# Performance work log

Hardware: AMD Instinct MI355X
Metric: run time of the kernel (lower is better)

The kernel has to match this reference:

```python
import jax, jax.numpy as jnp
import numpy as np

B, L, D, H, HID = 2048, 512, 17, 8, 256  # batch, max entities, feat dim, heads, mlp hidden
SPECIAL, OUT = 9, 23  # special vector dims, policy logits (7+16)


def _lin(k, out_d, in_d, scale):
    kw, kb = jax.random.split(k)
    W = jax.random.normal(kw, (out_d, in_d), jnp.float32) * scale
    b = jax.random.normal(kb, (out_d,), jnp.float32) * 0.01
    return W, b


def setup_inputs() -> dict:
    key = jax.random.key(0)
    ks = jax.random.split(key, 16)
    # observations: row 0 holds the 9-dim special vector, rows 1..L are ragged entities
    x = jax.random.normal(ks[0], (B, L + 1, D), jnp.float32)
    lengths = jax.random.randint(ks[1], (B,), 1, L + 1)
    mask = (jnp.arange(L)[None, :] < lengths[:, None]).astype(jnp.float32)
    x = x.at[:, 1:, :].multiply(mask[:, :, None])  # zero rows mark padding
    s = 1.0 / np.sqrt(D)
    # per-head K/V projections (num_heads separate tiny Linears)
    Wk = jax.random.normal(ks[2], (H, D, D), jnp.float32) * s
    bk = jax.random.normal(ks[3], (H, D), jnp.float32) * 0.01
    Wv = jax.random.normal(ks[4], (H, D, D), jnp.float32) * s
    bv = jax.random.normal(ks[5], (H, D), jnp.float32) * 0.01
    q = jax.random.normal(ks[6], (H, D), jnp.float32)  # learned per-head queries
    Wo, bo = _lin(ks[7], D, H * D, 1.0 / np.sqrt(H * D))
    sc = 1.0 / np.sqrt(D + SPECIAL)
    pW1, pb1 = _lin(ks[8], HID, D + SPECIAL, sc)
    pW2, pb2 = _lin(ks[9], HID, HID, 1.0 / np.sqrt(HID))
    pW3, pb3 = _lin(ks[10], OUT, HID, 1.0 / np.sqrt(HID))
    vW1, vb1 = _lin(ks[11], HID, D + SPECIAL, sc)
    vW2, vb2 = _lin(ks[12], HID, HID, 1.0 / np.sqrt(HID))
    vW3, vb3 = _lin(ks[13], 1, HID, 1.0 / np.sqrt(HID))
    return dict(x=x, Wk=Wk, bk=bk, Wv=Wv, bv=bv, q=q, Wo=Wo, bo=bo,
                pW1=pW1, pb1=pb1, pW2=pW2, pb2=pb2, pW3=pW3, pb3=pb3,
                vW1=vW1, vb1=vb1, vW2=vW2, vb2=vb2, vW3=vW3, vb3=vb3)


def _mlp(h, W1, b1, W2, b2, W3, b3):
    h = jax.nn.relu(h @ W1.T + b1)
    h = jax.nn.relu(h @ W2.T + b2)
    return h @ W3.T + b3


def reference(x, Wk, bk, Wv, bv, q, Wo, bo,
              pW1, pb1, pW2, pb2, pW3, pb3,
              vW1, vb1, vW2, vb2, vW3, vb3):
    special = x[:, 0, :SPECIAL]            # [B, 9]
    seq = x[:, 1:, :]                      # [B, L, D]
    mask = jnp.sum(jnp.abs(seq), axis=-1) != 0  # [B, L] non-padded rows
    # per-head keys/values for all samples at once (batched over the head loop)
    keys = jnp.einsum('bld,hed->bhle', seq, Wk) + bk[None, :, None, :]   # [B,H,L,D]
    vals = jnp.einsum('bld,hed->bhle', seq, Wv) + bv[None, :, None, :]   # [B,H,L,D]
    scores = jnp.einsum('bhle,he->bhl', keys, q)                          # [B,H,L]
    scores = jnp.where(mask[:, None, :], scores, -1e9)
    w = jax.nn.softmax(scores, axis=-1)                                   # [B,H,L]
    agg = jnp.einsum('bhl,bhle->bhe', w, vals).reshape(x.shape[0], H * D)  # concat heads
    attn = agg @ Wo.T + bo                                                # [B, D]
    comb = jnp.concatenate([attn, special], axis=-1)                      # [B, D+9]
    logits = _mlp(comb, pW1, pb1, pW2, pb2, pW3, pb3)                     # [B, 23]
    value = _mlp(comb, vW1, vb1, vW2, vb2, vW3, vb3)                      # [B, 1]
    return logits, value
```

## Files before the change

kernel.cpp:

```cpp
#include <hip/hip_runtime.h>
#include <hip/hip_bf16.h>

#define B_ 2048
#define D_ 17
#define H_ 8
#define HID_ 256
#define OUT_ 23
#define XROW 8721

__device__ __forceinline__ float4 ld4u(const float* p) {
  float4 v; __builtin_memcpy(&v, p, 16); return v;
}
__device__ __forceinline__ float bclane(float v, int l) {
  return __uint_as_float(__builtin_amdgcn_readlane(__float_as_uint(v), l));
}

__global__ __launch_bounds__(256) void prep_kernel(
    const float* __restrict__ pW2, const float* __restrict__ vW2,
    const float* __restrict__ Wk, const float* __restrict__ bk,
    const float* __restrict__ q,
    float* __restrict__ pW2t, float* __restrict__ vW2t, float* __restrict__ qkc)
{
  const int bid = blockIdx.x;
  const int t = threadIdx.x;
  if (bid == 128) {
    if (t < H_ * D_) {
      const int h = t / D_, dd = t - h * D_;
      float s = 0.f;
      #pragma unroll
      for (int e = 0; e < D_; ++e) s = fmaf(Wk[h*289 + e*D_ + dd], q[h*D_ + e], s);
      qkc[h*18 + dd] = s;
    } else if (t < H_ * D_ + H_) {
      const int h = t - H_ * D_;
      float s = 0.f;
      #pragma unroll
      for (int e = 0; e < D_; ++e) s = fmaf(bk[h*D_ + e], q[h*D_ + e], s);
      qkc[h*18 + 17] = s;
    }
    return;
  }
  __shared__ float tile[32][33];
  const int m = bid >> 6, tid = bid & 63;
  const int ti = (tid >> 3) * 32, tk = (tid & 7) * 32;
  const float* src = m ? vW2 : pW2;
  float* dst = m ? vW2t : pW2t;
  const int tx = t & 31, ty = t >> 5;
  #pragma unroll
  for (int r = 0; r < 4; ++r) tile[ty + 8*r][tx] = src[(ti + ty + 8*r)*HID_ + tk + tx];
  __syncthreads();
  #pragma unroll
  for (int r = 0; r < 4; ++r) dst[(tk + ty + 8*r)*HID_ + ti + tx] = tile[tx][ty + 8*r];
}

__global__ __launch_bounds__(64) void attn_part_kernel(
    const float* __restrict__ x, const float* __restrict__ qkc,
    float* __restrict__ part)
{
  const int bid = blockIdx.x;
  const int b = bid >> 2, q = bid & 3;
  const int lane = threadIdx.x;
  const int h = lane & 7, rg = lane >> 3;
  const float* xs = x + (size_t)b * XROW + D_;
  const int r0 = q * 128;

  const float w0 = xs[(size_t)(r0 + 8 * (lane & 15)) * D_];
  const unsigned long long lv = __ballot((lane < 16) && (w0 != 0.f));
  const int nch = lv ? (64 - __builtin_clzll(lv)) : 0;

  float qk[D_];
  #pragma unroll
  for (int d = 0; d < D_; ++d) qk[d] = qkc[h*18 + d];
  const float chr = qkc[h*18 + 17];

  float den = 0.f, acc[D_];
  #pragma unroll
  for (int d = 0; d < D_; ++d) acc[d] = 0.f;

  if (nch) {
    const float* rb = xs + (size_t)(r0 + rg) * D_;
    float4 A0, A1, A2, A3; float A4;
    float4 C0, C1, C2, C3; float C4;
    auto loadA = [&](int g) {
      const float* rp = rb + g * 136;
      A0 = ld4u(rp); A1 = ld4u(rp+4); A2 = ld4u(rp+8); A3 = ld4u(rp+12); A4 = rp[16];
    };
    auto loadC = [&](int g) {
      const float* rp = rb + g * 136;
      C0 = ld4u(rp); C1 = ld4u(rp+4); C2 = ld4u(rp+8); C3 = ld4u(rp+12); C4 = rp[16];
    };
    auto comp = [&](const float4& v0, const float4& v1, const float4& v2, const float4& v3, float v4) {
      float sc = chr;
      sc = fmaf(qk[0],  v0.x, sc); sc = fmaf(qk[1],  v0.y, sc);
      sc = fmaf(qk[2],  v0.z, sc); sc = fmaf(qk[3],  v0.w, sc);
      sc = fmaf(qk[4],  v1.x, sc); sc = fmaf(qk[5],  v1.y, sc);
      sc = fmaf(qk[6],  v1.z, sc); sc = fmaf(qk[7],  v1.w, sc);
      sc = fmaf(qk[8],  v2.x, sc); sc = fmaf(qk[9],  v2.y, sc);
      sc = fmaf(qk[10], v2.z, sc); sc = fmaf(qk[11], v2.w, sc);
      sc = fmaf(qk[12], v3.x, sc); sc = fmaf(qk[13], v3.y, sc);
      sc = fmaf(qk[14], v3.z, sc); sc = fmaf(qk[15], v3.w, sc);
      sc = fmaf(qk[16], v4, sc);
      const float p = (v0.x != 0.f) ? __expf(sc) : 0.f;
      den += p;
      acc[0]  = fmaf(p, v0.x, acc[0]);  acc[1]  = fmaf(p, v0.y, acc[1]);
      acc[2]  = fmaf(p, v0.z, acc[2]);  acc[3]  = fmaf(p, v0.w, acc[3]);
      acc[4]  = fmaf(p, v1.x, acc[4]);  acc[5]  = fmaf(p, v1.y, acc[5]);
      acc[6]  = fmaf(p, v1.z, acc[6]);  acc[7]  = fmaf(p, v1.w, acc[7]);
      acc[8]  = fmaf(p, v2.x, acc[8]);  acc[9]  = fmaf(p, v2.y, acc[9]);
      acc[10] = fmaf(p, v2.z, acc[10]); acc[11] = fmaf(p, v2.w, acc[11]);
      acc[12] = fmaf(p, v3.x, acc[12]); acc[13] = fmaf(p, v3.y, acc[13]);
      acc[14] = fmaf(p, v3.z, acc[14]); acc[15] = fmaf(p, v3.w, acc[15]);
      acc[16] = fmaf(p, v4, acc[16]);
    };

    loadA(0);
    #pragma unroll 1
    for (int g = 0; g < nch; g += 2) {
      if (g + 1 < nch) loadC(g + 1);
      comp(A0, A1, A2, A3, A4);
      if (g + 1 >= nch) break;
      if (g + 2 < nch) loadA(g + 2);
      comp(C0, C1, C2, C3, C4);
    }
  }

  #pragma unroll
  for (int m = 8; m <= 32; m <<= 1) {
    den += __shfl_xor(den, m, 64);
    #pragma unroll
    for (int d = 0; d < D_; ++d) acc[d] += __shfl_xor(acc[d], m, 64);
  }
  if (lane < 8) {
    float* pp = part + (size_t)bid * 144 + lane * 18;
    pp[0] = den;
    #pragma unroll
    for (int d = 0; d < D_; ++d) pp[1 + d] = acc[d];
  }
}

__global__ __launch_bounds__(512) void mlp_fused_kernel(
    const float* __restrict__ x, const float* __restrict__ part,
    const float* __restrict__ Wv, const float* __restrict__ bv,
    const float* __restrict__ Wo, const float* __restrict__ bo,
    const float* __restrict__ pW1, const float* __restrict__ pb1,
    const float* __restrict__ pW2t, const float* __restrict__ pb2,
    const float* __restrict__ pW3, const float* __restrict__ pb3,
    const float* __restrict__ vW1, const float* __restrict__ vb1,
    const float* __restrict__ vW2t, const float* __restrict__ vb2,
    const float* __restrict__ vW3, const float* __restrict__ vb3,
    float* __restrict__ out)
{
  __shared__ float s_swn[8][136];
  __shared__ float s_agg[8][136];
  __shared__ float s_wp[8][136];
  __shared__ float s_comb[8][26];
  __shared__ __align__(16) float s_red[2][3][8][HID_];
  __shared__ __align__(16) float s_h2[2][8][HID_];

  const int t = threadIdx.x;
  const int b0 = blockIdx.x * 8;
  const int cb = t >> 6;
  const int cl = t & 63;

  {
    const float* pb_ = part + (size_t)(b0 + cb) * 4 * 144;
    for (int u = cl; u < 136; u += 64) {
      const int hh = u / D_, d = u - hh * D_;
      const float dn = pb_[hh*18] + pb_[144 + hh*18] + pb_[288 + hh*18] + pb_[432 + hh*18];
      const float ac = pb_[hh*18+1+d] + pb_[144 + hh*18+1+d] + pb_[288 + hh*18+1+d] + pb_[432 + hh*18+1+d];
      s_swn[cb][u] = ac / dn;
    }
  }
  __syncthreads();
  for (int u = cl; u < 136; u += 64) {
    const int hh = u / D_, e = u - hh * D_;
    float s = bv[u];
    #pragma unroll
    for (int d = 0; d < D_; ++d) s = fmaf(Wv[hh*289 + e*D_ + d], s_swn[cb][hh*D_ + d], s);
    s_agg[cb][u] = s;
  }
  __syncthreads();
  for (int u = cl; u < 136; u += 64) {
    const int o = u >> 3, pt = u & 7;
    float s = 0.f;
    #pragma unroll
    for (int j = 0; j < D_; ++j) s = fmaf(Wo[o*136 + pt*D_ + j], s_agg[cb][pt*D_ + j], s);
    s_wp[cb][u] = s;
  }
  __syncthreads();
  if (cl < D_) {
    float s = bo[cl];
    #pragma unroll
    for (int pt = 0; pt < 8; ++pt) s += s_wp[cb][cl*8 + pt];
    s_comb[cb][cl] = s;
  } else if (cl < 26) {
    s_comb[cb][cl] = x[(size_t)(b0 + cb) * XROW + (cl - D_)];
  }
  __syncthreads();

  const int p = t >> 8;
  const int kq = (t >> 6) & 3;
  const int ln = t & 63;
  const float* W1  = p ? vW1  : pW1;   const float* B1 = p ? vb1 : pb1;
  const float* W2t = p ? vW2t : pW2t;  const float* B2 = p ? vb2 : pb2;

  float h[8];
  {
    const int i = kq * 64 + ln;
    float a[8];
    #pragma unroll
    for (int bb = 0; bb < 8; ++bb) a[bb] = 0.f;
    const float* wr = W1 + i * 26;
    for (int k = 0; k < 26; ++k) {
      const float wk = wr[k];
      #pragma unroll
      for (int bb = 0; bb < 8; ++bb) a[bb] = fmaf(wk, s_comb[bb][k], a[bb]);
    }
    const float bias = B1[i];
    #pragma unroll
    for (int bb = 0; bb < 8; ++bb) h[bb] = fmaxf(a[bb] + bias, 0.f);
  }

  float4 acc[8];
  #pragma unroll
  for (int bb = 0; bb < 8; ++bb) acc[bb] = make_float4(0.f, 0.f, 0.f, 0.f);
  {
    const float* wbase = W2t + (size_t)(kq * 64) * HID_ + 4 * ln;
    #pragma unroll 8
    for (int jj = 0; jj < 64; ++jj) {
      const float4 wv = *(const float4*)(wbase + (size_t)jj * HID_);
      #pragma unroll
      for (int bb = 0; bb < 8; ++bb) {
        const float hv = bclane(h[bb], jj);
        acc[bb].x = fmaf(wv.x, hv, acc[bb].x);
        acc[bb].y = fmaf(wv.y, hv, acc[bb].y);
        acc[bb].z = fmaf(wv.z, hv, acc[bb].z);
        acc[bb].w = fmaf(wv.w, hv, acc[bb].w);
      }
    }
  }
  if (kq > 0) {
    #pragma unroll
    for (int bb = 0; bb < 8; ++bb) *(float4*)&s_red[p][kq - 1][bb][4 * ln] = acc[bb];
  }
  __syncthreads();
  if (kq == 0) {
    const float4 bias = *(const float4*)&B2[4 * ln];
    #pragma unroll
    for (int bb = 0; bb < 8; ++bb) {
      const float4 r0 = *(const float4*)&s_red[p][0][bb][4 * ln];
      const float4 r1 = *(const float4*)&s_red[p][1][bb][4 * ln];
      const float4 r2 = *(const float4*)&s_red[p][2][bb][4 * ln];
      float4 r;
      r.x = fmaxf(acc[bb].x + r0.x + r1.x + r2.x + bias.x, 0.f);
      r.y = fmaxf(acc[bb].y + r0.y + r1.y + r2.y + bias.y, 0.f);
      r.z = fmaxf(acc[bb].z + r0.z + r1.z + r2.z + bias.z, 0.f);
      r.w = fmaxf(acc[bb].w + r0.w + r1.w + r2.w + bias.w, 0.f);
      *(float4*)&s_h2[p][bb][4 * ln] = r;
    }
  }
  __syncthreads();

  if (t < 184) {
    const int bb = t / OUT_, o = t - bb * OUT_;
    const float4* w4 = (const float4*)(pW3 + o * HID_);
    const float4* h4 = (const float4*)&s_h2[0][bb][0];
    float s = pb3[o];
    for (int k = 0; k < 64; ++k) {
      const float4 wv = w4[k], hv = h4[k];
      s = fmaf(wv.x, hv.x, fmaf(wv.y, hv.y, fmaf(wv.z, hv.z, fmaf(wv.w, hv.w, s))));
    }
    out[(size_t)(b0 + bb) * OUT_ + o] = s;
  } else if (t >= 256 && t < 264) {
    const int bb = t - 256;
    const float4* w4 = (const float4*)vW3;
    const float4* h4 = (const float4*)&s_h2[1][bb][0];
    float s = vb3[0];
    for (int k = 0; k < 64; ++k) {
      const float4 wv = w4[k], hv = h4[k];
      s = fmaf(wv.x, hv.x, fmaf(wv.y, hv.y, fmaf(wv.z, hv.z, fmaf(wv.w, hv.w, s))));
    }
    out[(size_t)B_ * OUT_ + b0 + bb] = s;
  }
}

extern "C" void kernel_launch(void* const* d_in, const int* in_sizes, int n_in,
                              void* d_out, int out_size, void* d_ws, size_t ws_size,
                              hipStream_t stream) {
  (void)in_sizes; (void)n_in; (void)out_size; (void)ws_size;
  const float* x   = (const float*)d_in[0];
  const float* Wk  = (const float*)d_in[1];
  const float* bk  = (const float*)d_in[2];
  const float* Wv  = (const float*)d_in[3];
  const float* bv  = (const float*)d_in[4];
  const float* q   = (const float*)d_in[5];
  const float* Wo  = (const float*)d_in[6];
  const float* bo  = (const float*)d_in[7];
  const float* pW1 = (const float*)d_in[8];
  const float* pb1 = (const float*)d_in[9];
  const float* pW2 = (const float*)d_in[10];
  const float* pb2 = (const float*)d_in[11];
  const float* pW3 = (const float*)d_in[12];
  const float* pb3 = (const float*)d_in[13];
  const float* vW1 = (const float*)d_in[14];
  const float* vb1 = (const float*)d_in[15];
  const float* vW2 = (const float*)d_in[16];
  const float* vb2 = (const float*)d_in[17];
  const float* vW3 = (const float*)d_in[18];
  const float* vb3 = (const float*)d_in[19];
  float* out = (float*)d_out;

  float* pW2t = (float*)d_ws;
  float* vW2t = pW2t + (size_t)HID_ * HID_;
  float* qkc  = vW2t + (size_t)HID_ * HID_;
  float* part = qkc + 160;

  prep_kernel<<<129, 256, 0, stream>>>(pW2, vW2, Wk, bk, q, pW2t, vW2t, qkc);
  attn_part_kernel<<<B_ * 4, 64, 0, stream>>>(x, qkc, part);
  mlp_fused_kernel<<<B_ / 8, 512, 0, stream>>>(x, part, Wv, bv, Wo, bo,
                                               pW1, pb1, pW2t, pb2, pW3, pb3,
                                               vW1, vb1, vW2t, vb2, vW3, vb3, out);
}
```

Before: 57.38 us.

## Interleave attention row chunks across four waves per sample with ballot early exit

The attention partial kernel now launches one 256-thread block per sample instead of four 64-thread blocks that each took a contiguous quarter of the rows. Each wave takes 8-row chunks strided by four, so all waves share the valid prefix of a ragged sample instead of trailing quarters sitting idle. The upfront ballot that sized each block's chunk count is replaced by a per-chunk ballot that breaks once a chunk is entirely padding. This aims to balance work across waves for ragged lengths and cut idle blocks. The cost is more ballots in the loop, and a launch bound of 6 that may restrict registers.

```diff
diff --git a/kernel.cpp b/kernel.cpp
--- a/kernel.cpp
+++ b/kernel.cpp
@@ -52,20 +52,15 @@
   for (int r = 0; r < 4; ++r) dst[(tk + ty + 8*r)*HID_ + ti + tx] = tile[tx][ty + 8*r];
 }
 
-__global__ __launch_bounds__(64) void attn_part_kernel(
+__global__ __launch_bounds__(256, 6) void attn_part_kernel(
     const float* __restrict__ x, const float* __restrict__ qkc,
     float* __restrict__ part)
 {
-  const int bid = blockIdx.x;
-  const int b = bid >> 2, q = bid & 3;
-  const int lane = threadIdx.x;
+  const int b = blockIdx.x;
+  const int t = threadIdx.x;
+  const int w = t >> 6, lane = t & 63;
   const int h = lane & 7, rg = lane >> 3;
   const float* xs = x + (size_t)b * XROW + D_;
-  const int r0 = q * 128;
-
-  const float w0 = xs[(size_t)(r0 + 8 * (lane & 15)) * D_];
-  const unsigned long long lv = __ballot((lane < 16) && (w0 != 0.f));
-  const int nch = lv ? (64 - __builtin_clzll(lv)) : 0;
 
   float qk[D_];
   #pragma unroll
@@ -76,51 +71,51 @@
   #pragma unroll
   for (int d = 0; d < D_; ++d) acc[d] = 0.f;
 
-  if (nch) {
-    const float* rb = xs + (size_t)(r0 + rg) * D_;
-    float4 A0, A1, A2, A3; float A4;
-    float4 C0, C1, C2, C3; float C4;
-    auto loadA = [&](int g) {
-      const float* rp = rb + g * 136;
-      A0 = ld4u(rp); A1 = ld4u(rp+4); A2 = ld4u(rp+8); A3 = ld4u(rp+12); A4 = rp[16];
-    };
-    auto loadC = [&](int g) {
-      const float* rp = rb + g * 136;
-      C0 = ld4u(rp); C1 = ld4u(rp+4); C2 = ld4u(rp+8); C3 = ld4u(rp+12); C4 = rp[16];
-    };
-    auto comp = [&](const float4& v0, const float4& v1, const float4& v2, const float4& v3, float v4) {
-      float sc = chr;
-      sc = fmaf(qk[0],  v0.x, sc); sc = fmaf(qk[1],  v0.y, sc);
-      sc = fmaf(qk[2],  v0.z, sc); sc = fmaf(qk[3],  v0.w, sc);
-      sc = fmaf(qk[4],  v1.x, sc); sc = fmaf(qk[5],  v1.y, sc);
-      sc = fmaf(qk[6],  v1.z, sc); sc = fmaf(qk[7],  v1.w, sc);
-      sc = fmaf(qk[8],  v2.x, sc); sc = fmaf(qk[9],  v2.y, sc);
-      sc = fmaf(qk[10], v2.z, sc); sc = fmaf(qk[11], v2.w, sc);
-      sc = fmaf(qk[12], v3.x, sc); sc = fmaf(qk[13], v3.y, sc);
-      sc = fmaf(qk[14], v3.z, sc); sc = fmaf(qk[15], v3.w, sc);
-      sc = fmaf(qk[16], v4, sc);
-      const float p = (v0.x != 0.f) ? __expf(sc) : 0.f;
-      den += p;
-      acc[0]  = fmaf(p, v0.x, acc[0]);  acc[1]  = fmaf(p, v0.y, acc[1]);
-      acc[2]  = fmaf(p, v0.z, acc[2]);  acc[3]  = fmaf(p, v0.w, acc[3]);
-      acc[4]  = fmaf(p, v1.x, acc[4]);  acc[5]  = fmaf(p, v1.y, acc[5]);
-      acc[6]  = fmaf(p, v1.z, acc[6]);  acc[7]  = fmaf(p, v1.w, acc[7]);
-      acc[8]  = fmaf(p, v2.x, acc[8]);  acc[9]  = fmaf(p, v2.y, acc[9]);
-      acc[10] = fmaf(p, v2.z, acc[10]); acc[11] = fmaf(p, v2.w, acc[11]);
-      acc[12] = fmaf(p, v3.x, acc[12]); acc[13] = fmaf(p, v3.y, acc[13]);
-      acc[14] = fmaf(p, v3.z, acc[14]); acc[15] = fmaf(p, v3.w, acc[15]);
-      acc[16] = fmaf(p, v4, acc[16]);
-    };
-
-    loadA(0);
-    #pragma unroll 1
-    for (int g = 0; g < nch; g += 2) {
-      if (g + 1 < nch) loadC(g + 1);
-      comp(A0, A1, A2, A3, A4);
-      if (g + 1 >= nch) break;
-      if (g + 2 < nch) loadA(g + 2);
-      comp(C0, C1, C2, C3, C4);
-    }
+  const float* rb = xs + (size_t)rg * D_;
+  float4 A0, A1, A2, A3; float A4;
+  float4 C0, C1, C2, C3; float C4;
+  auto loadA = [&](int c) {
+    const float* rp = rb + c * 136;
+    A0 = ld4u(rp); A1 = ld4u(rp+4); A2 = ld4u(rp+8); A3 = ld4u(rp+12); A4 = rp[16];
+  };
+  auto loadC = [&](int c) {
+    const float* rp = rb + c * 136;
+    C0 = ld4u(rp); C1 = ld4u(rp+4); C2 = ld4u(rp+8); C3 = ld4u(rp+12); C4 = rp[16];
+  };
+  auto comp = [&](const float4& v0, const float4& v1, const float4& v2, const float4& v3, float v4) {
+    float sc = chr;
+    sc = fmaf(qk[0],  v0.x, sc); sc = fmaf(qk[1],  v0.y, sc);
+    sc = fmaf(qk[2],  v0.z, sc); sc = fmaf(qk[3],  v0.w, sc);
+    sc = fmaf(qk[4],  v1.x, sc); sc = fmaf(qk[5],  v1.y, sc);
+    sc = fmaf(qk[6],  v1.z, sc); sc = fmaf(qk[7],  v1.w, sc);
+    sc = fmaf(qk[8],  v2.x, sc); sc = fmaf(qk[9],  v2.y, sc);
+    sc = fmaf(qk[10], v2.z, sc); sc = fmaf(qk[11], v2.w, sc);
+    sc = fmaf(qk[12], v3.x, sc); sc = fmaf(qk[13], v3.y, sc);
+    sc = fmaf(qk[14], v3.z, sc); sc = fmaf(qk[15], v3.w, sc);
+    sc = fmaf(qk[16], v4, sc);
+    const float p = (v0.x != 0.f) ? __expf(sc) : 0.f;
+    den += p;
+    acc[0]  = fmaf(p, v0.x, acc[0]);  acc[1]  = fmaf(p, v0.y, acc[1]);
+    acc[2]  = fmaf(p, v0.z, acc[2]);  acc[3]  = fmaf(p, v0.w, acc[3]);
+    acc[4]  = fmaf(p, v1.x, acc[4]);  acc[5]  = fmaf(p, v1.y, acc[5]);
+    acc[6]  = fmaf(p, v1.z, acc[6]);  acc[7]  = fmaf(p, v1.w, acc[7]);
+    acc[8]  = fmaf(p, v2.x, acc[8]);  acc[9]  = fmaf(p, v2.y, acc[9]);
+    acc[10] = fmaf(p, v2.z, acc[10]); acc[11] = fmaf(p, v2.w, acc[11]);
+    acc[12] = fmaf(p, v3.x, acc[12]); acc[13] = fmaf(p, v3.y, acc[13]);
+    acc[14] = fmaf(p, v3.z, acc[14]); acc[15] = fmaf(p, v3.w, acc[15]);
+    acc[16] = fmaf(p, v4, acc[16]);
+  };
+
+  loadA(w);
+  #pragma unroll 1
+  for (int c = w; c < 64; c += 8) {
+    if (c + 4 < 64) loadC(c + 4);
+    if (__ballot(A0.x != 0.f) == 0ull) break;
+    comp(A0, A1, A2, A3, A4);
+    if (c + 4 >= 64) break;
+    if (c + 8 < 64) loadA(c + 8);
+    if (__ballot(C0.x != 0.f) == 0ull) break;
+    comp(C0, C1, C2, C3, C4);
   }
 
   #pragma unroll
@@ -130,7 +125,7 @@
     for (int d = 0; d < D_; ++d) acc[d] += __shfl_xor(acc[d], m, 64);
   }
   if (lane < 8) {
-    float* pp = part + (size_t)bid * 144 + lane * 18;
+    float* pp = part + ((size_t)b * 4 + w) * 144 + lane * 18;
     pp[0] = den;
     #pragma unroll
     for (int d = 0; d < D_; ++d) pp[1 + d] = acc[d];
@@ -315,7 +310,7 @@
   float* part = qkc + 160;
 
   prep_kernel<<<129, 256, 0, stream>>>(pW2, vW2, Wk, bk, q, pW2t, vW2t, qkc);
-  attn_part_kernel<<<B_ * 4, 64, 0, stream>>>(x, qkc, part);
+  attn_part_kernel<<<B_, 256, 0, stream>>>(x, qkc, part);
   mlp_fused_kernel<<<B_ / 8, 512, 0, stream>>>(x, part, Wv, bv, Wo, bo,
                                                pW1, pb1, pW2t, pb2, pW3, pb3,
                                                vW1, vb1, vW2t, vb2, vW3, vb3, out);
```

Result: slower. 64.71 us (+12.8%).
